# Performance work log

Hardware: AMD Instinct MI355X
Metric: run time of the kernel (lower is better)

## Reference

```python
import jax, jax.numpy as jnp
import numpy as np
from jax import lax

B, T, L = 2048, 80, 128


def setup_inputs() -> dict:
    key = jax.random.key(0)
    k1, k2, k3, k4, k5 = jax.random.split(key, 5)
    x = jax.random.normal(k1, (B, T, L), dtype=jnp.float32)  # emissions (model logits)
    y = jax.random.randint(k2, (B, T), 0, L)                 # gold tag sequence
    trans = jax.random.normal(k3, (L, L), dtype=jnp.float32) * 0.1
    start_trans = jax.random.normal(k4, (L,), dtype=jnp.float32) * 0.1
    end_trans = jax.random.normal(k5, (L,), dtype=jnp.float32) * 0.1
    return {"x": x, "trans": trans, "start_trans": start_trans,
            "end_trans": end_trans, "y": y}


def reference(x, trans, start_trans, end_trans, y):
    # Linear-chain CRF log-likelihood (TorchCRF semantics, mask = all ones).
    # x: [B,T,L] emissions, y: [B,T] gold tags. Returns [B] log-likelihoods.
    # --- numerator: score of the gold path ---
    emit = jnp.take_along_axis(x, y[..., None], axis=2).squeeze(-1).sum(axis=1)  # [B]
    tr = trans[y[:, :-1], y[:, 1:]].sum(axis=1)                                  # [B]
    numerator = start_trans[y[:, 0]] + emit + tr + end_trans[y[:, -1]]           # [B]
    # --- denominator: log-partition via forward algorithm (scan over time) ---
    alpha0 = start_trans[None, :] + x[:, 0]  # [B,L]
    xt = jnp.swapaxes(x, 0, 1)[1:]           # [T-1,B,L]

    def step(alpha, h_t):
        # alpha[b,i] + trans[i,j] -> logsumexp over i, then add emission h_t[b,j]
        a = jax.nn.logsumexp(alpha[:, :, None] + trans[None, :, :], axis=1) + h_t
        return a, None

    alpha, _ = lax.scan(step, alpha0, xt)
    log_z = jax.nn.logsumexp(alpha + end_trans[None, :], axis=1)  # [B]
    return numerator - log_z
```

## Files before the change

kernel.cpp:

```cpp
#include <hip/hip_runtime.h>
#include <math.h>


#define CRF_B 2048
#define CRF_T 80
#define CRF_L 128

typedef __attribute__((ext_vector_type(8))) short bf16x8_t;
typedef __attribute__((ext_vector_type(4))) float f32x4_t;

__device__ __forceinline__ int pack_bf16_trunc(float lo, float hi) {
    return (int)((__float_as_uint(lo) >> 16) | (__float_as_uint(hi) & 0xFFFF0000u));
}
__device__ __forceinline__ unsigned short bft(float f) {
    return (unsigned short)(__float_as_uint(f) >> 16);
}

__global__ __launch_bounds__(128, 1) void crf_v9_kernel(
    const float* __restrict__ x,
    const float* __restrict__ trans,
    const float* __restrict__ start_trans,
    const float* __restrict__ end_trans,
    const int*   __restrict__ y,
    float* __restrict__ out)
{
    const int tid  = threadIdx.x;
    const int w    = tid >> 6;
    const int lane = tid & 63;
    const int q    = lane >> 4;
    const int a    = lane & 15;
    const int row0 = blockIdx.x * 4;
    const int brow = row0 + (a & 3);

    __shared__ __attribute__((aligned(16))) float u_lds[4][132];
    __shared__ float crunB_lds[4];
    __shared__ float numb[4];

    #pragma unroll
    for (int rr = 0; rr < 2; ++rr) {
        const int bb = row0 + 2 * w + rr;
        const int* yb = y + bb * CRF_T;
        const float* xbn = x + (size_t)bb * CRF_T * CRF_L;
        float p = 0.f;
        for (int t = lane; t < CRF_T; t += 64) {
            const int yt = yb[t];
            p += xbn[t * CRF_L + yt];
            p += (t + 1 < CRF_T) ? trans[yt * CRF_L + yb[t + 1]] : end_trans[yt];
            if (t == 0) p += start_trans[yt];
        }
        #pragma unroll
        for (int off = 1; off <= 32; off <<= 1) p += __shfl_xor(p, off);
        if (lane == 0) numb[2 * w + rr] = p;
    }

    bf16x8_t Afr[8][4];
    {
        const int out_lo = 32 * (a >> 2) + (a & 3);
        const int in_lo  = 32 * q;
        const int so = w ? CRF_L : 1;
        const int si = w ? 1 : CRF_L;
        #pragma unroll
        for (int mt = 0; mt < 8; ++mt) {
            const int ob = (out_lo + 4 * mt) * so;
            #pragma unroll
            for (int kk = 0; kk < 4; ++kk) {
                union { bf16x8_t v; unsigned short s[8]; } u;
                #pragma unroll
                for (int j = 0; j < 8; ++j) {
                    const int in_s = in_lo + 8 * kk + j;
                    u.s[j] = bft(__expf(trans[ob + in_s * si]));
                }
                Afr[mt][kk] = u.v;
            }
        }
    }

    const float* xr = x + (size_t)brow * CRF_T * CRF_L;
    int tcur = w ? 78 : 1;
    const int tstep = w ? -1 : 1;

    float P[8][4];
    bf16x8_t Bfr[4];
    {
        const float* bias = w ? end_trans : start_trans;
        const float* xp = xr + (size_t)(w ? 79 : 0) * CRF_L + 32 * q;
        const float* bp = bias + 32 * q;
        #pragma unroll
        for (int mt = 0; mt < 8; ++mt) {
            const f32x4_t bv = *(const f32x4_t*)&bp[4 * mt];
            const f32x4_t xv = *(const f32x4_t*)&xp[4 * mt];
            #pragma unroll
            for (int r = 0; r < 4; ++r) P[mt][r] = __expf(bv[r] + xv[r]);
        }
        #pragma unroll
        for (int kk = 0; kk < 4; ++kk) {
            union { bf16x8_t v; int wd[4]; } u;
            u.wd[0] = pack_bf16_trunc(P[2 * kk][0],     P[2 * kk][1]);
            u.wd[1] = pack_bf16_trunc(P[2 * kk][2],     P[2 * kk][3]);
            u.wd[2] = pack_bf16_trunc(P[2 * kk + 1][0], P[2 * kk + 1][1]);
            u.wd[3] = pack_bf16_trunc(P[2 * kk + 1][2], P[2 * kk + 1][3]);
            Bfr[kk] = u.v;
        }
    }

    f32x4_t xc[8], xn[8];
    {
        const float* xp = xr + (size_t)tcur * CRF_L + 32 * q;
        #pragma unroll
        for (int mt = 0; mt < 8; ++mt) xc[mt] = *(const f32x4_t*)&xp[4 * mt];
    }

    float crun = 0.f, inv = 1.f, Mv = 1.f;

#define CRF_STEP(MEASURE, APPLY, LAST) do {                                     \
        if (!(LAST)) {                                                          \
            const float* xp_ = xr + (size_t)(tcur + tstep) * CRF_L + 32 * q;    \
            _Pragma("unroll")                                                   \
            for (int mt = 0; mt < 8; ++mt) xn[mt] = *(const f32x4_t*)&xp_[4*mt];\
        }                                                                       \
        if (APPLY) { crun += __logf(Mv); inv = __builtin_amdgcn_rcpf(Mv); }     \
        float e_[8][4];                                                         \
        _Pragma("unroll")                                                       \
        for (int mt = 0; mt < 8; ++mt)                                          \
            _Pragma("unroll")                                                   \
            for (int r = 0; r < 4; ++r) {                                       \
                float v_ = __expf(xc[mt][r]);                                   \
                if (APPLY) v_ *= inv;                                           \
                e_[mt][r] = v_;                                                 \
            }                                                                   \
        _Pragma("unroll")                                                       \
        for (int mt = 0; mt < 8; ++mt) {                                        \
            f32x4_t a_ = {0.f, 0.f, 0.f, 0.f};                                  \
            _Pragma("unroll")                                                   \
            for (int kk = 0; kk < 4; ++kk)                                      \
                a_ = __builtin_amdgcn_mfma_f32_16x16x32_bf16(Afr[mt][kk],       \
                                                             Bfr[kk], a_,      \
                                                             0, 0, 0);         \
            _Pragma("unroll")                                                   \
            for (int r = 0; r < 4; ++r) P[mt][r] = a_[r] * e_[mt][r];           \
        }                                                                       \
        _Pragma("unroll")                                                       \
        for (int kk = 0; kk < 4; ++kk) {                                        \
            union { bf16x8_t v; int wd[4]; } u_;                                \
            u_.wd[0] = pack_bf16_trunc(P[2 * kk][0],     P[2 * kk][1]);         \
            u_.wd[1] = pack_bf16_trunc(P[2 * kk][2],     P[2 * kk][3]);         \
            u_.wd[2] = pack_bf16_trunc(P[2 * kk + 1][0], P[2 * kk + 1][1]);     \
            u_.wd[3] = pack_bf16_trunc(P[2 * kk + 1][2], P[2 * kk + 1][3]);     \
            Bfr[kk] = u_.v;                                                     \
        }                                                                       \
        if (MEASURE) {                                                          \
            float g_ = P[0][0];                                                 \
            _Pragma("unroll")                                                   \
            for (int mt = 0; mt < 8; ++mt)                                      \
                _Pragma("unroll")                                               \
                for (int r = 0; r < 4; ++r) g_ = fmaxf(g_, P[mt][r]);           \
            g_ = fmaxf(g_, __shfl_xor(g_, 4));                                  \
            g_ = fmaxf(g_, __shfl_xor(g_, 8));                                  \
            g_ = fmaxf(g_, __shfl_xor(g_, 16));                                 \
            g_ = fmaxf(g_, __shfl_xor(g_, 32));                                 \
            Mv = g_;                                                            \
        }                                                                       \
        if (!(LAST)) {                                                          \
            _Pragma("unroll")                                                   \
            for (int mt = 0; mt < 8; ++mt) xc[mt] = xn[mt];                     \
            tcur += tstep;                                                      \
        }                                                                       \
    } while (0)

    for (int k4 = 0; k4 < 9; ++k4) {
        CRF_STEP(0, 0, 0);
        CRF_STEP(0, 0, 0);
        CRF_STEP(1, 0, 0);
        CRF_STEP(0, 1, 0);
    }
    CRF_STEP(0, 0, 0);
    CRF_STEP(0, 0, 0);
    CRF_STEP(0, 0, 1);
#undef CRF_STEP

    if (w == 1) {
        #pragma unroll
        for (int mt = 0; mt < 8; ++mt) {
            f32x4_t a_ = {0.f, 0.f, 0.f, 0.f};
            #pragma unroll
            for (int kk = 0; kk < 4; ++kk)
                a_ = __builtin_amdgcn_mfma_f32_16x16x32_bf16(Afr[mt][kk],
                                                             Bfr[kk], a_,
                                                             0, 0, 0);
            if (a < 4)
                *(f32x4_t*)&u_lds[a][32 * q + 4 * mt] = a_;
        }
        if (a < 4 && q == 0) crunB_lds[a] = crun;
    }
    __syncthreads();
    if (w == 0) {
        float s = 0.f;
        #pragma unroll
        for (int mt = 0; mt < 8; ++mt) {
            const f32x4_t uv = *(const f32x4_t*)&u_lds[a & 3][32 * q + 4 * mt];
            #pragma unroll
            for (int r = 0; r < 4; ++r) s += P[mt][r] * uv[r];
        }
        s += __shfl_xor(s, 4);
        s += __shfl_xor(s, 8);
        s += __shfl_xor(s, 16);
        s += __shfl_xor(s, 32);
        if (a < 4 && q == 0)
            out[row0 + a] = numb[a] - (crun + crunB_lds[a] + __logf(s * 0.25f));
    }
}

extern "C" void kernel_launch(void* const* d_in, const int* in_sizes, int n_in,
                              void* d_out, int out_size, void* d_ws, size_t ws_size,
                              hipStream_t stream) {
    const float* x     = (const float*)d_in[0];
    const float* trans = (const float*)d_in[1];
    const float* st    = (const float*)d_in[2];
    const float* et    = (const float*)d_in[3];
    const int*   y     = (const int*)d_in[4];
    float* out = (float*)d_out;

    crf_v9_kernel<<<CRF_B / 4, 128, 0, stream>>>(x, trans, st, et, y, out);
}
```

Before: 168.7 us.

## Halve batch rows per block and split MFMA accumulation chains

Each block now handles 2 batch rows instead of 4, doubling the grid to 1024 blocks, and launch bounds allow 2 blocks per CU. The serial MFMA accumulation over K is split into two independent accumulators that are summed afterwards, shortening the dependency chain in the latency-bound recurrence. The MFMA N dimension now replicates each row 8 times instead of 4, so more of the matrix-core work is redundant. The occupancy hint of 2 may also constrain registers for the large Afr fragment array.

```diff
diff --git a/kernel.cpp b/kernel.cpp
--- a/kernel.cpp
+++ b/kernel.cpp
@@ -16,7 +16,7 @@
     return (unsigned short)(__float_as_uint(f) >> 16);
 }
 
-__global__ __launch_bounds__(128, 1) void crf_v9_kernel(
+__global__ __launch_bounds__(128, 2) void crf_v10_kernel(
     const float* __restrict__ x,
     const float* __restrict__ trans,
     const float* __restrict__ start_trans,
@@ -29,16 +29,15 @@
     const int lane = tid & 63;
     const int q    = lane >> 4;
     const int a    = lane & 15;
-    const int row0 = blockIdx.x * 4;
-    const int brow = row0 + (a & 3);
-
-    __shared__ __attribute__((aligned(16))) float u_lds[4][132];
-    __shared__ float crunB_lds[4];
-    __shared__ float numb[4];
-
-    #pragma unroll
-    for (int rr = 0; rr < 2; ++rr) {
-        const int bb = row0 + 2 * w + rr;
+    const int row0 = blockIdx.x * 2;
+    const int brow = row0 + (a & 1);
+
+    __shared__ __attribute__((aligned(16))) float u_lds[2][132];
+    __shared__ float crunB_lds[2];
+    __shared__ float numb[2];
+
+    {
+        const int bb = row0 + w;
         const int* yb = y + bb * CRF_T;
         const float* xbn = x + (size_t)bb * CRF_T * CRF_L;
         float p = 0.f;
@@ -50,7 +49,7 @@
         }
         #pragma unroll
         for (int off = 1; off <= 32; off <<= 1) p += __shfl_xor(p, off);
-        if (lane == 0) numb[2 * w + rr] = p;
+        if (lane == 0) numb[w] = p;
     }
 
     bf16x8_t Afr[8][4];
@@ -130,14 +129,19 @@
             }                                                                   \
         _Pragma("unroll")                                                       \
         for (int mt = 0; mt < 8; ++mt) {                                        \
-            f32x4_t a_ = {0.f, 0.f, 0.f, 0.f};                                  \
-            _Pragma("unroll")                                                   \
-            for (int kk = 0; kk < 4; ++kk)                                      \
-                a_ = __builtin_amdgcn_mfma_f32_16x16x32_bf16(Afr[mt][kk],       \
-                                                             Bfr[kk], a_,      \
-                                                             0, 0, 0);         \
-            _Pragma("unroll")                                                   \
-            for (int r = 0; r < 4; ++r) P[mt][r] = a_[r] * e_[mt][r];           \
+            f32x4_t c0 = {0.f, 0.f, 0.f, 0.f};                                  \
+            f32x4_t c1 = {0.f, 0.f, 0.f, 0.f};                                  \
+            c0 = __builtin_amdgcn_mfma_f32_16x16x32_bf16(Afr[mt][0], Bfr[0],    \
+                                                         c0, 0, 0, 0);         \
+            c1 = __builtin_amdgcn_mfma_f32_16x16x32_bf16(Afr[mt][1], Bfr[1],    \
+                                                         c1, 0, 0, 0);         \
+            c0 = __builtin_amdgcn_mfma_f32_16x16x32_bf16(Afr[mt][2], Bfr[2],    \
+                                                         c0, 0, 0, 0);         \
+            c1 = __builtin_amdgcn_mfma_f32_16x16x32_bf16(Afr[mt][3], Bfr[3],    \
+                                                         c1, 0, 0, 0);         \
+            _Pragma("unroll")                                                   \
+            for (int r = 0; r < 4; ++r)                                         \
+                P[mt][r] = (c0[r] + c1[r]) * e_[mt][r];                         \
         }                                                                       \
         _Pragma("unroll")                                                       \
         for (int kk = 0; kk < 4; ++kk) {                                        \
@@ -154,6 +158,7 @@
             for (int mt = 0; mt < 8; ++mt)                                      \
                 _Pragma("unroll")                                               \
                 for (int r = 0; r < 4; ++r) g_ = fmaxf(g_, P[mt][r]);           \
+            g_ = fmaxf(g_, __shfl_xor(g_, 2));                                  \
             g_ = fmaxf(g_, __shfl_xor(g_, 4));                                  \
             g_ = fmaxf(g_, __shfl_xor(g_, 8));                                  \
             g_ = fmaxf(g_, __shfl_xor(g_, 16));                                 \
@@ -181,32 +186,34 @@
     if (w == 1) {
         #pragma unroll
         for (int mt = 0; mt < 8; ++mt) {
-            f32x4_t a_ = {0.f, 0.f, 0.f, 0.f};
-            #pragma unroll
-            for (int kk = 0; kk < 4; ++kk)
-                a_ = __builtin_amdgcn_mfma_f32_16x16x32_bf16(Afr[mt][kk],
-                                                             Bfr[kk], a_,
-                                                             0, 0, 0);
-            if (a < 4)
-                *(f32x4_t*)&u_lds[a][32 * q + 4 * mt] = a_;
-        }
-        if (a < 4 && q == 0) crunB_lds[a] = crun;
+            f32x4_t c0 = {0.f, 0.f, 0.f, 0.f};
+            f32x4_t c1 = {0.f, 0.f, 0.f, 0.f};
+            c0 = __builtin_amdgcn_mfma_f32_16x16x32_bf16(Afr[mt][0], Bfr[0], c0, 0, 0, 0);
+            c1 = __builtin_amdgcn_mfma_f32_16x16x32_bf16(Afr[mt][1], Bfr[1], c1, 0, 0, 0);
+            c0 = __builtin_amdgcn_mfma_f32_16x16x32_bf16(Afr[mt][2], Bfr[2], c0, 0, 0, 0);
+            c1 = __builtin_amdgcn_mfma_f32_16x16x32_bf16(Afr[mt][3], Bfr[3], c1, 0, 0, 0);
+            if (a < 2) {
+                f32x4_t uv;
+                #pragma unroll
+                for (int r = 0; r < 4; ++r) uv[r] = c0[r] + c1[r];
+                *(f32x4_t*)&u_lds[a][32 * q + 4 * mt] = uv;
+            }
+        }
+        if (a < 2 && q == 0) crunB_lds[a] = crun;
     }
     __syncthreads();
     if (w == 0) {
         float s = 0.f;
         #pragma unroll
         for (int mt = 0; mt < 8; ++mt) {
-            const f32x4_t uv = *(const f32x4_t*)&u_lds[a & 3][32 * q + 4 * mt];
+            const f32x4_t uv = *(const f32x4_t*)&u_lds[a & 1][32 * q + 4 * mt];
             #pragma unroll
             for (int r = 0; r < 4; ++r) s += P[mt][r] * uv[r];
         }
-        s += __shfl_xor(s, 4);
-        s += __shfl_xor(s, 8);
         s += __shfl_xor(s, 16);
         s += __shfl_xor(s, 32);
-        if (a < 4 && q == 0)
-            out[row0 + a] = numb[a] - (crun + crunB_lds[a] + __logf(s * 0.25f));
+        if (a < 2 && q == 0)
+            out[row0 + a] = numb[a] - (crun + crunB_lds[a] + __logf(s));
     }
 }
 
@@ -220,5 +227,5 @@
     const int*   y     = (const int*)d_in[4];
     float* out = (float*)d_out;
 
-    crf_v9_kernel<<<CRF_B / 4, 128, 0, stream>>>(x, trans, st, et, y, out);
-}
+    crf_v10_kernel<<<CRF_B / 2, 128, 0, stream>>>(x, trans, st, et, y, out);
+}
```

New measurement: 261.7 us. 1.55x slower.
